# Kernel optimization log

Measured on AMD Instinct MI355X. Metric: run time of the kernel, lower is better.

Reference implementation:

```python
import jax, jax.numpy as jnp
import numpy as np

DIM = 1792      # 256+512+1024 = WRN50 layer1-3 channels
GAMMA_D = 1
K_TOP = 3
EPS = 0.1
MAX_ITER = 200
B, H, W = 2, 56, 56


def avg_pool3x3(x):
    # F.avg_pool2d(x, 3, 1, 1), count_include_pad=True -> always divide by 9
    s = jax.lax.reduce_window(x, 0.0, jax.lax.add, (1, 1, 3, 3), (1, 1, 1, 1),
                              [(0, 0), (0, 0), (1, 1), (1, 1)])
    return s / 9.0


def descriptor(p1, p2, p3, w_coord, b_coord, w_eca):
    sample = avg_pool3x3(p1)
    b, _, h, w = sample.shape
    for o in (p2, p3):
        o = avg_pool3x3(o)
        # F.interpolate(..., mode='bilinear', align_corners=False) == half-pixel bilinear
        o = jax.image.resize(o, (o.shape[0], o.shape[1], h, w), method='bilinear')
        sample = jnp.concatenate([sample, o], axis=1)      # [b,1792,h,w]
    # CoordConv2d(dim, dim//gamma_d, 1): append normalized coord channels, 1x1 conv
    xx = jnp.broadcast_to(jnp.linspace(-1.0, 1.0, w, dtype=sample.dtype)[None, None, None, :], (b, 1, h, w))
    yy = jnp.broadcast_to(jnp.linspace(-1.0, 1.0, h, dtype=sample.dtype)[None, None, :, None], (b, 1, h, w))
    z = jnp.concatenate([sample, xx, yy], axis=1)          # [b,1794,h,w]
    phi = jnp.einsum('bchw,oc->bohw', z, w_coord) + b_coord[None, :, None, None]
    # eca_layer(dim, k_size=9): GAP -> conv1d over channel axis -> sigmoid gate
    y = phi.mean(axis=(2, 3))                              # [b,C]
    y = jax.lax.conv_general_dilated(y[:, None, :], w_eca[None, None, :], (1,),
                                     [(4, 4)], dimension_numbers=('NCH', 'OIH', 'NCH'))[:, 0, :]
    gate = jax.nn.sigmoid(y)[:, :, None, None]
    return phi * (1.0 + 0.1 * gate)                        # 0.1*eca(phi) + phi


def sinkhorn(Ccost, mu, nu):
    # plain Sinkhorn (TopK_custom forward), 200 iterations
    G = jnp.exp(-Ccost / EPS)                              # [bs,n,m]
    bs, n, m = Ccost.shape

    def body(i, uv):
        u, v = uv
        u = mu / (G * v).sum(-1, keepdims=True)            # [bs,n,1]
        v = nu / (G * u).sum(-2, keepdims=True)            # [bs,1,m]
        return (u, v)

    u0 = jnp.ones((bs, n, 1), Ccost.dtype)
    v0 = jnp.ones((bs, 1, m), Ccost.dtype) / m
    u, v = jax.lax.fori_loop(0, MAX_ITER, body, (u0, v0))
    return u * G * v


def soft_topk(scores):
    # SOFT top-k via 2-anchor optimal transport; selects the K_TOP SMALLEST scores
    bs, n = scores.shape
    anchors = jnp.array([0.0, 1.0], scores.dtype)          # [selected, rest]
    Ccost = (scores[..., None] - anchors) ** 2             # [bs,n,2]
    Ccost = Ccost / jax.lax.stop_gradient(Ccost.max())
    mu = jnp.ones((1, n, 1), scores.dtype) / n
    nu = jnp.array([K_TOP / n, (n - K_TOP) / n], scores.dtype).reshape(1, 1, 2)
    Gamma = sinkhorn(Ccost, mu, nu)
    return Gamma[..., 0] * n                               # soft top-K membership mask


def adfa_forward(p1, p2, p3, w_coord, b_coord, w_eca, C):
    phi = descriptor(p1, p2, p3, w_coord, b_coord, w_eca)  # [b,c,h,w]
    b, c, h, w = phi.shape
    phi_p = phi.reshape(b, c, h * w).transpose(0, 2, 1)    # [b,hw,c]
    # F.kl_div(log_softmax(phi_p), softmax(C^T)) = t*(log t - log q); summed, detached
    t = jax.nn.softmax(C.T, axis=-1)                       # [nC,c], nC == hw
    kl = t * (jnp.log(t) - jax.nn.log_softmax(phi_p, axis=-1))
    kldist = jax.lax.stop_gradient(kl.sum(axis=(1, 2), keepdims=True))  # [b,1,1]
    feat2 = (phi_p ** 2).sum(-1, keepdims=True)            # [b,hw,1]
    cent2 = (C ** 2).sum(0, keepdims=True)                 # [1,nC]
    dist = (feat2 + cent2 - 2.0 * (phi_p @ C)) * kldist    # [b,hw,nC]
    nC = dist.shape[-1]
    mask = soft_topk(dist.reshape(-1, nC)).reshape(dist.shape)
    d = (mask * dist).sum(-1, keepdims=True)               # [b,hw,1]
    # rearrange 'b (h w) c -> b c h w'
    return jnp.sqrt(d).reshape(b, h, w, 1).transpose(0, 3, 1, 2)  # [b,1,h,w]


def setup_inputs() -> dict:
    key = jax.random.key(0)
    ks = jax.random.split(key, 7)
    p1 = jax.random.normal(ks[0], (B, 256, H, W), jnp.float32)
    p2 = jax.random.normal(ks[1], (B, 512, H // 2, W // 2), jnp.float32)
    p3 = jax.random.normal(ks[2], (B, 1024, H // 4, W // 4), jnp.float32)
    fan_in = DIM + 2
    w_coord = jax.random.normal(ks[3], (DIM // GAMMA_D, fan_in), jnp.float32) / np.float32(np.sqrt(fan_in))
    b_coord = jax.random.normal(ks[4], (DIM // GAMMA_D,), jnp.float32) * 0.01
    w_eca = jax.random.normal(ks[5], (9,), jnp.float32) / 3.0
    C = jax.random.normal(ks[6], (DIM // GAMMA_D, H * W), jnp.float32) * 0.3
    return {"p1": p1, "p2": p2, "p3": p3, "w_coord": w_coord,
            "b_coord": b_coord, "w_eca": w_eca, "C": C}


def reference(p1, p2, p3, w_coord, b_coord, w_eca, C):
    return adfa_forward(p1, p2, p3, w_coord, b_coord, w_eca, C)
```

## Files before the change

### kernel.cpp

```cpp
#include <hip/hip_runtime.h>

#define HWn 3136
#define DIMc 1792
#define ZCc 1794
#define NBb 2
#define KP 1856
#define MP 3200

typedef unsigned short u16;
typedef unsigned int u32;
typedef unsigned char u8;
typedef short bf16x8 __attribute__((ext_vector_type(8)));
typedef float f32x4 __attribute__((ext_vector_type(4)));

#define GL_LDS(gp, lp) __builtin_amdgcn_global_load_lds(\
    (const __attribute__((address_space(1))) void*)(gp), \
    (__attribute__((address_space(3))) void*)(lp), 16, 0, 0)

__device__ __forceinline__ u16 f2b(float f) {
  u32 u = __float_as_uint(f);
  u32 r = (u + 0x7fffu + ((u >> 16) & 1u)) >> 16;
  return (u16)r;
}
__device__ __forceinline__ float b2f(u16 h) { return __uint_as_float((u32)h << 16); }

__device__ __forceinline__ u32 pk4_fp8(float a, float b, float c, float d) {
  u32 lo = __builtin_amdgcn_cvt_pk_fp8_f32(a, b, 0, false);
  return __builtin_amdgcn_cvt_pk_fp8_f32(c, d, lo, true);
}

__device__ __forceinline__ int xcd_swz(int orig, int nwg) {
  int q = nwg >> 3, r = nwg & 7;
  int xcd = orig & 7, j = orig >> 3;
  int base = (xcd < r) ? xcd * (q + 1) : r * (q + 1) + (xcd - r) * q;
  return base + j;
}

__device__ __forceinline__ float blkSum256(float v) {
  __shared__ float sh[4];
  #pragma unroll
  for (int o = 32; o > 0; o >>= 1) v += __shfl_xor(v, o, 64);
  int lane = threadIdx.x & 63, w = threadIdx.x >> 6;
  if (lane == 0) sh[w] = v;
  __syncthreads();
  float r = sh[0] + sh[1] + sh[2] + sh[3];
  __syncthreads();
  return r;
}
__device__ __forceinline__ float blkMax256(float v) {
  __shared__ float sh[4];
  #pragma unroll
  for (int o = 32; o > 0; o >>= 1) v = fmaxf(v, __shfl_xor(v, o, 64));
  int lane = threadIdx.x & 63, w = threadIdx.x >> 6;
  if (lane == 0) sh[w] = v;
  __syncthreads();
  float r = fmaxf(fmaxf(sh[0], sh[1]), fmaxf(sh[2], sh[3]));
  __syncthreads();
  return r;
}
__device__ __forceinline__ float blkMin256(float v) {
  __shared__ float sh[4];
  #pragma unroll
  for (int o = 32; o > 0; o >>= 1) v = fminf(v, __shfl_xor(v, o, 64));
  int lane = threadIdx.x & 63, w = threadIdx.x >> 6;
  if (lane == 0) sh[w] = v;
  __syncthreads();
  float r = fminf(fminf(sh[0], sh[1]), fminf(sh[2], sh[3]));
  __syncthreads();
  return r;
}

__global__ void pool_k(const float* __restrict__ in, float* __restrict__ out,
                       int total, int Hh, int Ww) {
  int idx = blockIdx.x * 256 + threadIdx.x;
  if (idx >= total) return;
  int w = idx % Ww; int h = (idx / Ww) % Hh; int bc = idx / (Ww * Hh);
  const float* p = in + (size_t)bc * Hh * Ww;
  float s = 0.f;
  #pragma unroll
  for (int dy = -1; dy <= 1; dy++) {
    int y = h + dy; if ((unsigned)y >= (unsigned)Hh) continue;
    #pragma unroll
    for (int dx = -1; dx <= 1; dx++) {
      int x = w + dx; if ((unsigned)x >= (unsigned)Ww) continue;
      s += p[y * Ww + x];
    }
  }
  out[idx] = s * (1.f / 9.f);
}

__device__ __forceinline__ float bilerp(const float* __restrict__ p, int Hin, int Win,
                                        int h, int w, float sc) {
  float fy = (h + 0.5f) * sc - 0.5f;
  float fx = (w + 0.5f) * sc - 0.5f;
  float y0f = floorf(fy), x0f = floorf(fx);
  int y0 = (int)y0f, x0 = (int)x0f;
  float wy = fy - y0f, wx = fx - x0f;
  int y0c = min(max(y0, 0), Hin - 1);
  int y1c = min(max(y0 + 1, 0), Hin - 1);
  int x0c = min(max(x0, 0), Win - 1);
  int x1c = min(max(x0 + 1, 0), Win - 1);
  float v00 = p[y0c * Win + x0c], v01 = p[y0c * Win + x1c];
  float v10 = p[y1c * Win + x0c], v11 = p[y1c * Win + x1c];
  return (1.f - wy) * ((1.f - wx) * v00 + wx * v01) + wy * ((1.f - wx) * v10 + wx * v11);
}

__global__ __launch_bounds__(256) void buildzt_k(const float* __restrict__ p1,
    const float* __restrict__ pp2, const float* __restrict__ pp3,
    u16* __restrict__ zt, float* __restrict__ psum) {
  __shared__ u16 tile[64][68];
  int b = blockIdx.z;
  int i0 = blockIdx.x * 64;
  int c0 = blockIdx.y * 64;
  int t = threadIdx.x;
  #pragma unroll
  for (int q = 0; q < 16; q++) {
    int idx = q * 256 + t;
    int cp = idx >> 6, ip = idx & 63;
    int cg = c0 + cp;
    int ig = i0 + ip;
    int h = ig / 56, w = ig % 56;
    float val;
    if (cg < 256) {
      const float* p = p1 + (size_t)(b * 256 + cg) * HWn;
      float s = 0.f;
      #pragma unroll
      for (int dy = -1; dy <= 1; dy++) {
        int y = h + dy; if ((unsigned)y >= 56u) continue;
        #pragma unroll
        for (int dx = -1; dx <= 1; dx++) {
          int x = w + dx; if ((unsigned)x >= 56u) continue;
          s += p[y * 56 + x];
        }
      }
      val = s * (1.f / 9.f);
    } else if (cg < 768) {
      val = bilerp(pp2 + (size_t)(b * 512 + (cg - 256)) * 784, 28, 28, h, w, 0.5f);
    } else if (cg < 1792) {
      val = bilerp(pp3 + (size_t)(b * 1024 + (cg - 768)) * 196, 14, 14, h, w, 0.25f);
    } else if (cg == 1792) {
      val = -1.f + (2.f / 55.f) * (float)w;
    } else if (cg == 1793) {
      val = -1.f + (2.f / 55.f) * (float)h;
    } else {
      val = 0.f;
    }
    tile[cp][ip] = f2b(val);
  }
  __syncthreads();
  #pragma unroll
  for (int q = 0; q < 4; q++) {
    int idx = q * 256 + t;
    int r2 = idx >> 4;
    int cc4 = (idx & 15) * 4;
    u32 lo = (u32)tile[cc4 + 0][r2] | ((u32)tile[cc4 + 1][r2] << 16);
    u32 hi = (u32)tile[cc4 + 2][r2] | ((u32)tile[cc4 + 3][r2] << 16);
    *reinterpret_cast<uint2*>(&zt[((size_t)b * MP + i0 + r2) * KP + c0 + cc4]) = make_uint2(lo, hi);
  }
  if (t < 64) {
    float s = 0.f;
    #pragma unroll 8
    for (int j = 0; j < 64; j++) s += b2f(tile[t][j]);
    psum[(((size_t)b * 29 + blockIdx.y) * 49 + blockIdx.x) * 64 + t] = s;
  }
}

__global__ void zred_k(const float* __restrict__ psum, float* __restrict__ zmean) {
  int cty = blockIdx.x, b = blockIdx.y;
  int t = threadIdx.x;
  float s = 0.f;
  for (int ix = 0; ix < 49; ix++)
    s += psum[(((size_t)b * 29 + cty) * 49 + ix) * 64 + t];
  zmean[b * KP + cty * 64 + t] = s * (1.f / (float)HWn);
}

__global__ __launch_bounds__(256) void yv_k(const u16* __restrict__ Wb, const float* __restrict__ zmean,
                                            const float* __restrict__ bias, float* __restrict__ yv) {
  __shared__ float zs[KP];
  int b = blockIdx.y;
  int o0 = blockIdx.x * 16;
  int t = threadIdx.x;
  for (int k = t; k < KP; k += 256) zs[k] = zmean[b * KP + k];
  __syncthreads();
  int w = t >> 6, l = t & 63;
  #pragma unroll
  for (int q = 0; q < 4; q++) {
    int o = o0 + w * 4 + q;
    const u16* R = Wb + (size_t)o * KP;
    float s = 0.f;
    for (int base = l * 8; base < KP; base += 512) {
      bf16x8 v = *reinterpret_cast<const bf16x8*>(&R[base]);
      #pragma unroll
      for (int j = 0; j < 8; j++) s += b2f((u16)v[j]) * zs[base + j];
    }
    #pragma unroll
    for (int off = 32; off > 0; off >>= 1) s += __shfl_xor(s, off, 64);
    if (l == 0) yv[b * DIMc + o] = s + bias[o];
  }
}

__global__ __launch_bounds__(256) void transC_k(const float* __restrict__ src, u16* __restrict__ dst,
                                                u8* __restrict__ dst8) {
  __shared__ u16 tile[64][68];
  int i0 = blockIdx.x * 64;
  int c0 = blockIdx.y * 64;
  int t = threadIdx.x;
  bool vi = (i0 < HWn);
  #pragma unroll
  for (int q = 0; q < 4; q++) {
    int idx = q * 256 + t;
    int r = idx >> 4;
    int c4 = (idx & 15) * 4;
    int sr = c0 + r;
    if (vi && sr < DIMc) {
      float4 rv = *reinterpret_cast<const float4*>(&src[(size_t)sr * HWn + i0 + c4]);
      tile[r][c4 + 0] = f2b(rv.x); tile[r][c4 + 1] = f2b(rv.y);
      tile[r][c4 + 2] = f2b(rv.z); tile[r][c4 + 3] = f2b(rv.w);
    } else {
      tile[r][c4 + 0] = 0; tile[r][c4 + 1] = 0; tile[r][c4 + 2] = 0; tile[r][c4 + 3] = 0;
    }
  }
  __syncthreads();
  #pragma unroll
  for (int q = 0; q < 4; q++) {
    int idx = q * 256 + t;
    int r2 = idx >> 4;
    int cc4 = (idx & 15) * 4;
    u16 e0 = tile[cc4 + 0][r2], e1 = tile[cc4 + 1][r2];
    u16 e2 = tile[cc4 + 2][r2], e3 = tile[cc4 + 3][r2];
    u32 lo = (u32)e0 | ((u32)e1 << 16);
    u32 hi = (u32)e2 | ((u32)e3 << 16);
    *reinterpret_cast<uint2*>(&dst[(size_t)(i0 + r2) * KP + c0 + cc4]) = make_uint2(lo, hi);
    u32 p8 = pk4_fp8(b2f(e0), b2f(e1), b2f(e2), b2f(e3));
    *reinterpret_cast<u32*>(&dst8[(size_t)(i0 + r2) * KP + c0 + cc4]) = p8;
  }
}

__global__ void convW_k(const float* __restrict__ Wc, u16* __restrict__ Wb) {
  int idx = blockIdx.x * 256 + threadIdx.x;
  const int total = DIMc * KP;
  if (idx >= total) return;
  int k = idx % KP, m = idx / KP;
  Wb[idx] = (k < ZCc) ? f2b(Wc[(size_t)m * ZCc + k]) : (u16)0;
}

#define STAGEF(buf, koff) { _Pragma("unroll") for (int j = 0; j < 2; j++) { \
    GL_LDS(gA[j] + (koff), &lA[buf][(j * 256 + tid) * 8]); \
    GL_LDS(gB[j] + (koff), &lB[buf][(j * 256 + tid) * 8]); } }

__global__ __launch_bounds__(256, 5) void gemmPhi_k(
    const u16* __restrict__ A, const u16* __restrict__ B,
    int ntN, int NT,
    const float* __restrict__ bias, const float* __restrict__ fac,
    u16* __restrict__ PhiOut) {
  __shared__ u16 lA[2][128 * 32];
  __shared__ u16 lB[2][128 * 32];
  int tid = threadIdx.x;
  int wid = tid >> 6, lane = tid & 63;
  int wm = wid >> 1, wn = wid & 1;
  int orig = blockIdx.x;
  int wg = xcd_swz(orig, gridDim.x);
  int mt = wg / ntN, nt = wg % ntN;
  int m0 = mt * 128, n0 = nt * 128;
  int rbase = tid >> 2;
  int srcX = ((tid & 3) ^ ((rbase >> 1) & 3)) * 8;
  const u16* gA[2]; const u16* gB[2];
  #pragma unroll
  for (int j = 0; j < 2; j++) {
    int rr = j * 64 + rbase;
    gA[j] = A + (size_t)(m0 + rr) * KP + srcX;
    gB[j] = B + (size_t)(n0 + rr) * KP + srcX;
  }
  int kq8 = (lane >> 4) * 8;
  int lr = lane & 15;
  f32x4 acc[4][4] = {};
  STAGEF(0, 0);
  __syncthreads();
  for (int t = 0; t < NT; t++) {
    int cur = t & 1;
    if (t + 1 < NT) STAGEF(cur ^ 1, (t + 1) * 32);
    bf16x8 af[4], bfr[4];
    #pragma unroll
    for (int f = 0; f < 4; f++) {
      int aR = wm * 64 + f * 16 + lr;
      af[f] = *reinterpret_cast<const bf16x8*>(
          &lA[cur][aR * 32 + (kq8 ^ (((aR >> 1) & 3) << 3))]);
    }
    #pragma unroll
    for (int g = 0; g < 4; g++) {
      int bR = wn * 64 + g * 16 + lr;
      bfr[g] = *reinterpret_cast<const bf16x8*>(
          &lB[cur][bR * 32 + (kq8 ^ (((bR >> 1) & 3) << 3))]);
    }
    #pragma unroll
    for (int f = 0; f < 4; f++)
      #pragma unroll
      for (int g = 0; g < 4; g++)
        acc[f][g] = __builtin_amdgcn_mfma_f32_16x16x32_bf16(af[f], bfr[g], acc[f][g], 0, 0, 0);
    __syncthreads();
  }
  int mbase = m0 + wm * 64 + (lane >> 4) * 4;
  int nbase = n0 + wn * 64 + lr;
  int bz0 = m0 / MP;
  float bvv[4], fcv[4];
  #pragma unroll
  for (int ni = 0; ni < 4; ni++) {
    int n = nbase + ni * 16;
    bvv[ni] = bias[n];
    fcv[ni] = fac[bz0 * DIMc + n];
  }
  #pragma unroll
  for (int mi = 0; mi < 4; mi++) {
    #pragma unroll
    for (int ni = 0; ni < 4; ni++) {
      int n = nbase + ni * 16;
      #pragma unroll
      for (int r = 0; r < 4; r++) {
        int m = mbase + mi * 16 + r;
        PhiOut[(size_t)m * KP + n] = f2b((acc[mi][ni][r] + bvv[ni]) * fcv[ni]);
      }
    }
  }
}

#define STAGE8(buf, koff) { \
    GL_LDS(gA8 + (koff), &lA[buf][tid * 16]); \
    GL_LDS(gB8 + (koff), &lB[buf][tid * 16]); }

__global__ __launch_bounds__(256, 5) void gemmD8_k(
    const u8* __restrict__ A, const u8* __restrict__ B,
    int ntN, int NT,
    const float* __restrict__ feat2, const float* __restrict__ cent2,
    const float* __restrict__ kld, u16* __restrict__ DistB,
    float* __restrict__ mmpart, int nblk) {
  __shared__ u8 lA[2][128 * 32];
  __shared__ u8 lB[2][128 * 32];
  int tid = threadIdx.x;
  int wid = tid >> 6, lane = tid & 63;
  int wm = wid >> 1, wn = wid & 1;
  int orig = blockIdx.x;
  int wg = xcd_swz(orig, gridDim.x);
  int mt = wg / ntN, nt = wg % ntN;
  int m0 = mt * 128, n0 = nt * 128;
  int row = tid >> 1;
  int srcOff = (((tid & 1) ^ ((tid >> 3) & 1)) << 4);
  const u8* gA8 = A + (size_t)(m0 + row) * KP + srcOff;
  const u8* gB8 = B + (size_t)(n0 + row) * KP + srcOff;
  int lr = lane & 15, c = lane >> 4;
  int off8 = ((((c >> 1) ^ ((lr >> 2) & 1)) << 4) | ((c & 1) << 3));
  int aoff = lr * 32 + off8;
  f32x4 acc[4][4] = {};
  STAGE8(0, 0);
  __syncthreads();
  for (int t = 0; t < NT; t++) {
    int cur = t & 1;
    if (t + 1 < NT) STAGE8(cur ^ 1, (t + 1) * 32);
    long av[4], bv[4];
    #pragma unroll
    for (int f = 0; f < 4; f++)
      av[f] = *reinterpret_cast<const long*>(&lA[cur][wm * 2048 + f * 512 + aoff]);
    #pragma unroll
    for (int g = 0; g < 4; g++)
      bv[g] = *reinterpret_cast<const long*>(&lB[cur][wn * 2048 + g * 512 + aoff]);
    #pragma unroll
    for (int f = 0; f < 4; f++)
      #pragma unroll
      for (int g = 0; g < 4; g++)
        acc[f][g] = __builtin_amdgcn_mfma_f32_16x16x32_fp8_fp8(av[f], bv[g], acc[f][g], 0, 0, 0);
    __syncthreads();
  }
  int mbase = m0 + wm * 64 + (lane >> 4) * 4;
  int nbase = n0 + wn * 64 + lr;
  float lmin = 3.4e38f, lmax = -3.4e38f;
  #pragma unroll
  for (int mi = 0; mi < 4; mi++) {
    int m = mbase + mi * 16;
    int bz = m / MP;
    int i = m - bz * MP;
    float kl = kld[bz];
    float f2r[4];
    #pragma unroll
    for (int r = 0; r < 4; r++)
      f2r[r] = (i + r < HWn) ? feat2[bz * HWn + i + r] : 0.f;
    #pragma unroll
    for (int ni = 0; ni < 4; ni++) {
      int n = nbase + ni * 16;
      if (n < HWn) {
        float c2 = cent2[n];
        #pragma unroll
        for (int r = 0; r < 4; r++) {
          if (i + r < HWn) {
            float dd = (f2r[r] + c2 - 2.f * acc[mi][ni][r]) * kl;
            DistB[((size_t)bz * HWn + i + r) * HWn + n] = f2b(dd);
            lmin = fminf(lmin, dd); lmax = fmaxf(lmax, dd);
          }
        }
      }
    }
  }
  #pragma unroll
  for (int o = 32; o > 0; o >>= 1) {
    lmin = fminf(lmin, __shfl_xor(lmin, o, 64));
    lmax = fmaxf(lmax, __shfl_xor(lmax, o, 64));
  }
  __syncthreads();
  float* scr = reinterpret_cast<float*>(&lA[0][0]);
  if (lane == 0) { scr[wid] = lmin; scr[4 + wid] = lmax; }
  __syncthreads();
  if (tid == 0) {
    mmpart[orig] = fminf(fminf(scr[0], scr[1]), fminf(scr[2], scr[3]));
    mmpart[nblk + orig] = fmaxf(fmaxf(scr[4], scr[5]), fmaxf(scr[6], scr[7]));
  }
}

__global__ void fac_k(const float* __restrict__ yv, const float* __restrict__ weca,
                      float* __restrict__ fac) {
  int idx = blockIdx.x * 256 + threadIdx.x;
  if (idx >= NBb * DIMc) return;
  int o = idx % DIMc; int b = idx / DIMc;
  float s = 0.f;
  #pragma unroll
  for (int k = 0; k < 9; k++) {
    int c = o + k - 4;
    if ((unsigned)c < (unsigned)DIMc) s += yv[b * DIMc + c] * weca[k];
  }
  fac[idx] = 1.f + 0.1f / (1.f + expf(-s));
}

__global__ __launch_bounds__(256) void rowfuse_k(const u16* __restrict__ Ct, u16* __restrict__ Phi,
    u8* __restrict__ Phi8, float* __restrict__ cent2,
    float* __restrict__ feat2, float* __restrict__ kpart) {
  int i = blockIdx.x;
  int t = threadIdx.x;
  if (i >= HWn) {
    if (t * 8 < KP) {
      #pragma unroll
      for (int b = 0; b < NBb; b++)
        *reinterpret_cast<uint2*>(&Phi8[((size_t)b * MP + i) * KP + t * 8]) = make_uint2(0, 0);
    }
    return;
  }
  bool act = (t * 8 < DIMc);
  const u16* R = Ct + (size_t)i * KP;
  float c[8];
  float mc = -3.4e38f, c2 = 0.f;
  if (act) {
    bf16x8 x = *reinterpret_cast<const bf16x8*>(&R[t * 8]);
    #pragma unroll
    for (int j = 0; j < 8; j++) {
      c[j] = b2f((u16)x[j]);
      mc = fmaxf(mc, c[j]);
      c2 += c[j] * c[j];
    }
  }
  mc = blkMax256(mc);
  float se = 0.f, sce = 0.f;
  float e[8];
  if (act) {
    #pragma unroll
    for (int j = 0; j < 8; j++) {
      e[j] = expf(c[j] - mc);
      se += e[j]; sce += e[j] * (c[j] - mc);
    }
  }
  se = blkSum256(se);
  sce = blkSum256(sce);
  c2 = blkSum256(c2);
  if (t == 0) cent2[i] = c2;
  float tl = sce / se - logf(se);
  float inv_se = 1.f / se;
  #pragma unroll
  for (int b = 0; b < NBb; b++) {
    u16* P = Phi + (size_t)b * MP * KP + (size_t)i * KP;
    u8* P8 = Phi8 + ((size_t)b * MP + i) * KP;
    float v[8];
    float mx = -3.4e38f;
    if (act) {
      bf16x8 x = *reinterpret_cast<const bf16x8*>(&P[t * 8]);
      #pragma unroll
      for (int j = 0; j < 8; j++) {
        v[j] = b2f((u16)x[j]);
        mx = fmaxf(mx, v[j]);
      }
      uint2 p8;
      p8.x = pk4_fp8(v[0], v[1], v[2], v[3]);
      p8.y = pk4_fp8(v[4], v[5], v[6], v[7]);
      *reinterpret_cast<uint2*>(&P8[t * 8]) = p8;
    } else if (t * 8 < KP) {
      bf16x8 zr = {};
      *reinterpret_cast<bf16x8*>(&P[t * 8]) = zr;
      *reinterpret_cast<uint2*>(&P8[t * 8]) = make_uint2(0, 0);
    }
    mx = blkMax256(mx);
    float sp = 0.f, f2 = 0.f, td = 0.f;
    if (act) {
      #pragma unroll
      for (int j = 0; j < 8; j++) {
        sp += expf(v[j] - mx);
        f2 += v[j] * v[j];
        td += e[j] * v[j];
      }
    }
    sp = blkSum256(sp);
    f2 = blkSum256(f2);
    td = blkSum256(td);
    if (t == 0) {
      feat2[b * HWn + i] = f2;
      kpart[b * HWn + i] = tl - td * inv_se + (mx + logf(sp));
    }
  }
}

__global__ __launch_bounds__(256) void kldred_k(const float* __restrict__ kpart, float* __restrict__ kld) {
  float s0 = 0.f, s1 = 0.f;
  for (int i = threadIdx.x; i < HWn; i += 256) { s0 += kpart[i]; s1 += kpart[HWn + i]; }
  s0 = blkSum256(s0); s1 = blkSum256(s1);
  if (threadIdx.x == 0) { kld[0] = s0; kld[1] = s1; }
}

__global__ __launch_bounds__(256) void mmred_k(const float* __restrict__ mmpart, float* __restrict__ gmm,
                                               int nblk) {
  float lmin = 3.4e38f, lmax = -3.4e38f;
  for (int i = threadIdx.x; i < nblk; i += 256) {
    lmin = fminf(lmin, mmpart[i]);
    lmax = fmaxf(lmax, mmpart[nblk + i]);
  }
  lmin = blkMin256(lmin); lmax = blkMax256(lmax);
  if (threadIdx.x == 0) { gmm[0] = lmin; gmm[1] = lmax; }
}

__global__ __launch_bounds__(256) void topk_k(const u16* __restrict__ dist,
    const float* __restrict__ gmm, float* __restrict__ out) {
  int lane = threadIdx.x & 63;
  int row = blockIdx.x * 4 + (threadIdx.x >> 6);
  const u16* dr = dist + (size_t)row * HWn;
  float gmin = gmm[0], gmax = gmm[1];
  float cmax = fmaxf(fmaxf(gmin * gmin, (gmin - 1.f) * (gmin - 1.f)),
                     fmaxf(gmax * gmax, (gmax - 1.f) * (gmax - 1.f)));
  float inv = 1.f / (0.1f * cmax);
  float rS[49];
  #pragma unroll
  for (int k = 0; k < 49; k++) {
    float dv = b2f(dr[k * 64 + lane]);
    rS[k] = expf((2.f * dv - 1.f) * inv);
  }
  const float nf = (float)HWn;
  float s = 1.f;
  for (int it = 0; it < 199; it++) {
    float loc = 0.f;
    #pragma unroll
    for (int k = 0; k < 49; k++)
      loc += __builtin_amdgcn_rcpf(fmaf(rS[k], s, 1.f));
    #pragma unroll
    for (int o = 32; o > 0; o >>= 1) loc += __shfl_xor(loc, o, 64);
    float snew = ((nf - 3.f) / 3.f) * loc * s / fmaxf(nf - loc, 1e-20f);
    float ds = fabsf(snew - s);
    s = snew;
    if (ds <= 1e-6f * fabsf(s)) break;
  }
  float A = 0.f, dl = 0.f;
  float hinv = 0.5f / inv;
  #pragma unroll
  for (int k = 0; k < 49; k++) {
    float w = 1.f / (1.f + rS[k] * s);
    A += w;
    float dv = fmaf(logf(rS[k]), hinv, 0.5f);
    dl += dv * w;
  }
  #pragma unroll
  for (int o = 32; o > 0; o >>= 1) { A += __shfl_xor(A, o, 64); dl += __shfl_xor(dl, o, 64); }
  float dsum = dl * (3.f / A);
  if (lane == 0) out[row] = sqrtf(fmaxf(dsum, 0.f));
}

extern "C" void kernel_launch(void* const* d_in, const int* in_sizes, int n_in,
                              void* d_out, int out_size, void* d_ws, size_t ws_size,
                              hipStream_t stream) {
  const float* p1 = (const float*)d_in[0];
  const float* p2 = (const float*)d_in[1];
  const float* p3 = (const float*)d_in[2];
  const float* wcoord = (const float*)d_in[3];
  const float* bcoord = (const float*)d_in[4];
  const float* weca = (const float*)d_in[5];
  const float* Cm = (const float*)d_in[6];
  float* out = (float*)d_out;
  float* ws = (float*)d_ws;

  u16*   zt    = (u16*)ws;
  float* pp2   = ws + 5939200;
  float* pp3   = ws + 6742016;
  u16*   dist  = (u16*)ws;
  u8*    phi8  = (u8*)(ws + 9834496);
  u8*    Ct8   = (u8*)(ws + 12804096);
  u16*   phi   = (u16*)(ws + 19668992);
  u16*   Ct    = (u16*)(ws + 25608192);
  u16*   Wb    = (u16*)(ws + 28577792);
  float* yv    = ws + 30240768;
  float* fac   = yv + 3584;
  float* feat2 = fac + 3584;
  float* cent2 = feat2 + 6272;
  float* kpart = cent2 + 3136;
  float* kld   = kpart + 6272;
  float* mmpart= kld + 2;
  float* gmm   = mmpart + 2500;
  float* zmean = gmm + 2;
  float* psum  = zmean + 3712;
  const int NBLK = 50 * 25;

  pool_k<<<3136, 256, 0, stream>>>(p2, pp2, NBb * 512 * 784, 28, 28);
  pool_k<<<1568, 256, 0, stream>>>(p3, pp3, NBb * 1024 * 196, 14, 14);
  buildzt_k<<<dim3(49, 29, NBb), 256, 0, stream>>>(p1, pp2, pp3, zt, psum);
  zred_k<<<dim3(29, NBb), 64, 0, stream>>>(psum, zmean);
  convW_k<<<(DIMc * KP + 255) / 256, 256, 0, stream>>>(wcoord, Wb);
  transC_k<<<dim3(50, 29, 1), 256, 0, stream>>>(Cm, Ct, Ct8);
  yv_k<<<dim3(DIMc / 16, NBb), 256, 0, stream>>>(Wb, zmean, bcoord, yv);
  fac_k<<<(NBb * DIMc + 255) / 256, 256, 0, stream>>>(yv, weca, fac);
  gemmPhi_k<<<50 * 14, 256, 0, stream>>>(zt, Wb, 14, 58, bcoord, fac, phi);
  rowfuse_k<<<MP, 256, 0, stream>>>(Ct, phi, phi8, cent2, feat2, kpart);
  kldred_k<<<1, 256, 0, stream>>>(kpart, kld);
  gemmD8_k<<<50 * 25, 256, 0, stream>>>(
      phi8, Ct8, 25, 56, feat2, cent2, kld, dist, mmpart, NBLK);
  mmred_k<<<1, 256, 0, stream>>>(mmpart, gmm, NBLK);
  topk_k<<<NBb * HWn / 4, 256, 0, stream>>>(dist, gmm, out);
}
```

Measured before the change: 293.1 us.

## Double fp8 GEMM K-tile to 64 with permuted K layout for 16-byte LDS reads

The fp8 distance GEMM now stages 64 bytes of K per iteration instead of 32, which halves the number of loop iterations and barriers. Each lane reads 16 bytes from LDS and feeds two MFMAs. The producers (transC_k and rowfuse_k) write the fp8 operands with a permuted K ordering so that each 16-byte chunk holds the two 8-byte MFMA operands in the right order. LDS use doubles to 32KB per block, which may lower occupancy under the launch bound of 5.

```diff
diff --git a/kernel.cpp b/kernel.cpp
--- a/kernel.cpp
+++ b/kernel.cpp
@@ -12,6 +12,7 @@
 typedef unsigned char u8;
 typedef short bf16x8 __attribute__((ext_vector_type(8)));
 typedef float f32x4 __attribute__((ext_vector_type(4)));
+typedef long lx2 __attribute__((ext_vector_type(2)));
 
 #define GL_LDS(gp, lp) __builtin_amdgcn_global_load_lds(\
     (const __attribute__((address_space(1))) void*)(gp), \
@@ -232,7 +233,9 @@
     u32 hi = (u32)e2 | ((u32)e3 << 16);
     *reinterpret_cast<uint2*>(&dst[(size_t)(i0 + r2) * KP + c0 + cc4]) = make_uint2(lo, hi);
     u32 p8 = pk4_fp8(b2f(e0), b2f(e1), b2f(e2), b2f(e3));
-    *reinterpret_cast<u32*>(&dst8[(size_t)(i0 + r2) * KP + c0 + cc4]) = p8;
+    int u = cc4 >> 3, half4 = (cc4 >> 2) & 1;
+    int up = ((u & 3) << 1) | (u >> 2);
+    *reinterpret_cast<u32*>(&dst8[(size_t)(i0 + r2) * KP + c0 + up * 8 + half4 * 4]) = p8;
   }
 }
 
@@ -323,9 +326,9 @@
   }
 }
 
-#define STAGE8(buf, koff) { \
-    GL_LDS(gA8 + (koff), &lA[buf][tid * 16]); \
-    GL_LDS(gB8 + (koff), &lB[buf][tid * 16]); }
+#define STAGE8(buf, koff) { _Pragma("unroll") for (int j = 0; j < 2; j++) { \
+    GL_LDS(gA8[j] + (koff), &lA[buf][j * 4096 + tid * 16]); \
+    GL_LDS(gB8[j] + (koff), &lB[buf][j * 4096 + tid * 16]); } }
 
 __global__ __launch_bounds__(256, 5) void gemmD8_k(
     const u8* __restrict__ A, const u8* __restrict__ B,
@@ -333,8 +336,8 @@
     const float* __restrict__ feat2, const float* __restrict__ cent2,
     const float* __restrict__ kld, u16* __restrict__ DistB,
     float* __restrict__ mmpart, int nblk) {
-  __shared__ u8 lA[2][128 * 32];
-  __shared__ u8 lB[2][128 * 32];
+  __shared__ u8 lA[2][128 * 64];
+  __shared__ u8 lB[2][128 * 64];
   int tid = threadIdx.x;
   int wid = tid >> 6, lane = tid & 63;
   int wm = wid >> 1, wn = wid & 1;
@@ -342,31 +345,38 @@
   int wg = xcd_swz(orig, gridDim.x);
   int mt = wg / ntN, nt = wg % ntN;
   int m0 = mt * 128, n0 = nt * 128;
-  int row = tid >> 1;
-  int srcOff = (((tid & 1) ^ ((tid >> 3) & 1)) << 4);
-  const u8* gA8 = A + (size_t)(m0 + row) * KP + srcOff;
-  const u8* gB8 = B + (size_t)(n0 + row) * KP + srcOff;
+  int rbase = tid >> 2;
+  int csrc = (((tid & 3) ^ ((rbase >> 1) & 3)) << 4);
+  const u8* gA8[2]; const u8* gB8[2];
+  #pragma unroll
+  for (int j = 0; j < 2; j++) {
+    int rr = j * 64 + rbase;
+    gA8[j] = A + (size_t)(m0 + rr) * KP + csrc;
+    gB8[j] = B + (size_t)(n0 + rr) * KP + csrc;
+  }
   int lr = lane & 15, c = lane >> 4;
-  int off8 = ((((c >> 1) ^ ((lr >> 2) & 1)) << 4) | ((c & 1) << 3));
-  int aoff = lr * 32 + off8;
+  int chunkoff = ((c ^ ((lr >> 1) & 3)) << 4);
+  int aoff = lr * 64 + chunkoff;
   f32x4 acc[4][4] = {};
   STAGE8(0, 0);
   __syncthreads();
   for (int t = 0; t < NT; t++) {
     int cur = t & 1;
-    if (t + 1 < NT) STAGE8(cur ^ 1, (t + 1) * 32);
-    long av[4], bv[4];
+    if (t + 1 < NT) STAGE8(cur ^ 1, (t + 1) * 64);
+    lx2 av[4], bv[4];
     #pragma unroll
     for (int f = 0; f < 4; f++)
-      av[f] = *reinterpret_cast<const long*>(&lA[cur][wm * 2048 + f * 512 + aoff]);
+      av[f] = *reinterpret_cast<const lx2*>(&lA[cur][wm * 4096 + f * 1024 + aoff]);
     #pragma unroll
     for (int g = 0; g < 4; g++)
-      bv[g] = *reinterpret_cast<const long*>(&lB[cur][wn * 2048 + g * 512 + aoff]);
+      bv[g] = *reinterpret_cast<const lx2*>(&lB[cur][wn * 4096 + g * 1024 + aoff]);
     #pragma unroll
     for (int f = 0; f < 4; f++)
       #pragma unroll
-      for (int g = 0; g < 4; g++)
-        acc[f][g] = __builtin_amdgcn_mfma_f32_16x16x32_fp8_fp8(av[f], bv[g], acc[f][g], 0, 0, 0);
+      for (int g = 0; g < 4; g++) {
+        acc[f][g] = __builtin_amdgcn_mfma_f32_16x16x32_fp8_fp8(av[f][0], bv[g][0], acc[f][g], 0, 0, 0);
+        acc[f][g] = __builtin_amdgcn_mfma_f32_16x16x32_fp8_fp8(av[f][1], bv[g][1], acc[f][g], 0, 0, 0);
+      }
     __syncthreads();
   }
   int mbase = m0 + wm * 64 + (lane >> 4) * 4;
@@ -432,11 +442,12 @@
     float* __restrict__ feat2, float* __restrict__ kpart) {
   int i = blockIdx.x;
   int t = threadIdx.x;
+  int tn = (t & ~7) | ((t & 3) << 1) | ((t >> 2) & 1);
   if (i >= HWn) {
     if (t * 8 < KP) {
       #pragma unroll
       for (int b = 0; b < NBb; b++)
-        *reinterpret_cast<uint2*>(&Phi8[((size_t)b * MP + i) * KP + t * 8]) = make_uint2(0, 0);
+        *reinterpret_cast<uint2*>(&Phi8[((size_t)b * MP + i) * KP + tn * 8]) = make_uint2(0, 0);
     }
     return;
   }
@@ -485,11 +496,11 @@
       uint2 p8;
       p8.x = pk4_fp8(v[0], v[1], v[2], v[3]);
       p8.y = pk4_fp8(v[4], v[5], v[6], v[7]);
-      *reinterpret_cast<uint2*>(&P8[t * 8]) = p8;
+      *reinterpret_cast<uint2*>(&P8[tn * 8]) = p8;
     } else if (t * 8 < KP) {
       bf16x8 zr = {};
       *reinterpret_cast<bf16x8*>(&P[t * 8]) = zr;
-      *reinterpret_cast<uint2*>(&P8[t * 8]) = make_uint2(0, 0);
+      *reinterpret_cast<uint2*>(&P8[tn * 8]) = make_uint2(0, 0);
     }
     mx = blkMax256(mx);
     float sp = 0.f, f2 = 0.f, td = 0.f;
@@ -619,7 +630,7 @@
   rowfuse_k<<<MP, 256, 0, stream>>>(Ct, phi, phi8, cent2, feat2, kpart);
   kldred_k<<<1, 256, 0, stream>>>(kpart, kld);
   gemmD8_k<<<50 * 25, 256, 0, stream>>>(
-      phi8, Ct8, 25, 56, feat2, cent2, kld, dist, mmpart, NBLK);
+      phi8, Ct8, 25, 28, feat2, cent2, kld, dist, mmpart, NBLK);
   mmred_k<<<1, 256, 0, stream>>>(mmpart, gmm, NBLK);
   topk_k<<<NBb * HWn / 4, 256, 0, stream>>>(dist, gmm, out);
 }
```

Result: faster. 275.9 us (-5.9%).
